# Kernel tuning notes

Measured on AMD Instinct MI355X. Metric: run time of the kernel, lower is better.

The kernel has to match this reference:

```python
import jax, jax.numpy as jnp
import numpy as np

N_NODES, N_EDGES = 512, 4096
P_OBJ, P_REL = 512, 256
D_NODE = D_EDGE = 256
H_GNN = 512
N_LAYERS = 2
N_OBJ_CLS, N_REL_CLS = 160, 26


def _pointnet(x, w1, b1, w2, b2, w3, b3):
    # x: [B, C_in, P] point cloud; pointwise conv1d == per-point MLP, then max-pool over points
    h = jax.nn.relu(jnp.einsum('bcp,cd->bpd', x, w1) + b1)
    h = jax.nn.relu(jnp.einsum('bpc,cd->bpd', h, w2) + b2)
    h = jnp.einsum('bpc,cd->bpd', h, w3) + b3
    return h.max(axis=1)  # [B, D]


def _mlp3(x, w1, b1, w2, b2, w3, b3):
    h = jax.nn.relu(x @ w1 + b1)
    h = jax.nn.relu(h @ w2 + b2)
    return h @ w3 + b3


def setup_inputs() -> dict:
    key = jax.random.key(0)
    ks = iter(jax.random.split(key, 64))

    def w(shape):
        fan = shape[-2]
        return jax.random.normal(next(ks), shape, dtype=jnp.float32) / np.float32(np.sqrt(fan))

    def b(shape):
        return jnp.zeros(shape, jnp.float32)

    d3 = 2 * D_NODE + D_EDGE  # triplet concat dim
    inp = dict(
        obj_points=jax.random.normal(next(ks), (N_NODES, 3, P_OBJ), dtype=jnp.float32),
        rel_points=jax.random.normal(next(ks), (N_EDGES, 4, P_REL), dtype=jnp.float32),
        edge_index=jax.random.randint(next(ks), (2, N_EDGES), 0, N_NODES),
        obj_w1=w((3, 64)), obj_b1=b((64,)), obj_w2=w((64, 128)), obj_b2=b((128,)),
        obj_w3=w((128, D_NODE)), obj_b3=b((D_NODE,)),
        rel_w1=w((4, 64)), rel_b1=b((64,)), rel_w2=w((64, 128)), rel_b2=b((128,)),
        rel_w3=w((128, D_EDGE)), rel_b3=b((D_EDGE,)),
        g_tw1=w((N_LAYERS, d3, H_GNN)), g_tb1=b((N_LAYERS, H_GNN)),
        g_tw2=w((N_LAYERS, H_GNN, d3)), g_tb2=b((N_LAYERS, d3)),
        g_nw1=w((N_LAYERS, D_NODE, H_GNN)), g_nb1=b((N_LAYERS, H_GNN)),
        g_nw2=w((N_LAYERS, H_GNN, D_NODE)), g_nb2=b((N_LAYERS, D_NODE)),
        oc_w1=w((D_NODE, 512)), oc_b1=b((512,)), oc_w2=w((512, 256)), oc_b2=b((256,)),
        oc_w3=w((256, N_OBJ_CLS)), oc_b3=b((N_OBJ_CLS,)),
        rc_w1=w((D_EDGE, 512)), rc_b1=b((512,)), rc_w2=w((512, 256)), rc_b2=b((256,)),
        rc_w3=w((256, N_REL_CLS)), rc_b3=b((N_REL_CLS,)),
    )
    return inp


def reference(obj_points, rel_points, edge_index,
              obj_w1, obj_b1, obj_w2, obj_b2, obj_w3, obj_b3,
              rel_w1, rel_b1, rel_w2, rel_b2, rel_w3, rel_b3,
              g_tw1, g_tb1, g_tw2, g_tb2, g_nw1, g_nb1, g_nw2, g_nb2,
              oc_w1, oc_b1, oc_w2, oc_b2, oc_w3, oc_b3,
              rc_w1, rc_b1, rc_w2, rc_b2, rc_w3, rc_b3):
    # PointNet encoders
    x = _pointnet(obj_points, obj_w1, obj_b1, obj_w2, obj_b2, obj_w3, obj_b3)  # [N, Dn]
    e = _pointnet(rel_points, rel_w1, rel_b1, rel_w2, rel_b2, rel_w3, rel_b3)  # [E, De]
    s, o = edge_index[0], edge_index[1]
    ones = jnp.ones((N_EDGES, 1), x.dtype)
    # Triplet GNN (GraphTripleConv-style message passing)
    for l in range(N_LAYERS):
        t = jnp.concatenate([x[s], e, x[o]], axis=-1)                 # [E, 2Dn+De]
        h = jax.nn.relu(t @ g_tw1[l] + g_tb1[l]) @ g_tw2[l] + g_tb2[l]
        ns = h[:, :D_NODE]
        ne = h[:, D_NODE:D_NODE + D_EDGE]
        no = h[:, D_NODE + D_EDGE:]
        pooled = (jax.ops.segment_sum(ns, s, num_segments=N_NODES)
                  + jax.ops.segment_sum(no, o, num_segments=N_NODES))
        cnt = (jax.ops.segment_sum(ones, s, num_segments=N_NODES)
               + jax.ops.segment_sum(ones, o, num_segments=N_NODES))
        avg = pooled / jnp.maximum(cnt, 1.0)                          # scatter-mean
        x = jax.nn.relu(avg @ g_nw1[l] + g_nb1[l]) @ g_nw2[l] + g_nb2[l]
        e = ne
    obj_cls = jax.nn.log_softmax(
        _mlp3(x, oc_w1, oc_b1, oc_w2, oc_b2, oc_w3, oc_b3), axis=-1)  # PointNetCls
    rel_cls = jax.nn.sigmoid(
        _mlp3(e, rc_w1, rc_b1, rc_w2, rc_b2, rc_w3, rc_b3))           # PointNetRelClsMulti
    return (obj_cls, rel_cls)
```

## Files before the change

kernel.cpp:

```cpp
#include <hip/hip_runtime.h>
#include <hip/hip_bf16.h>
#include <math.h>

#define N_NODES 512
#define N_EDGES 4096
#define D_NODE 256
#define D3 768
#define H_GNN 512
#define N_OBJ_CLS 160
#define N_REL_CLS 26

typedef __attribute__((ext_vector_type(8))) short bf16x8;
typedef __attribute__((ext_vector_type(4))) float f32x4;

__device__ __forceinline__ unsigned short f2bf(float x) {
  unsigned u = __float_as_uint(x);
  u = u + 0x7FFFu + ((u >> 16) & 1u);
  return (unsigned short)(u >> 16);
}
__device__ __forceinline__ float bf2f(unsigned short h) {
  return __uint_as_float(((unsigned)h) << 16);
}
__device__ __forceinline__ unsigned cvtpk(float a, float b) {
  __hip_bfloat162 h = __float22bfloat162_rn(make_float2(a, b));
  return *reinterpret_cast<unsigned*>(&h);
}

struct WEnt { const float* src; unsigned short* dh; unsigned short* dl; int K; int N; int start; };
struct WBatch { WEnt e[18]; int total; };

__global__ __launch_bounds__(256) void wtrans_batch(WBatch wb) {
  int idx = blockIdx.x * 256 + threadIdx.x;
  const int stride = gridDim.x * 256;
  for (; idx < wb.total; idx += stride) {
    int i = 0;
#pragma unroll
    for (int t = 1; t < 18; ++t) if (idx >= wb.e[t].start) i = t;
    const int local = idx - wb.e[i].start;
    const int K = wb.e[i].K;
    const int n = local / K, k = local - n * K;
    const float v = wb.e[i].src[k * wb.e[i].N + n];
    const unsigned short hi = f2bf(v);
    wb.e[i].dh[local] = hi;
    wb.e[i].dl[local] = f2bf(v - bf2f(hi));
  }
}

template<int CIN, int PTOT, int NSPLIT>
__global__ __launch_bounds__(256) void pointnet_mfma(
    const float* __restrict__ in,
    const float* __restrict__ w1, const float* __restrict__ b1,
    const unsigned short* __restrict__ w2t, const float* __restrict__ b2,
    const unsigned short* __restrict__ w3t, const float* __restrict__ b3,
    unsigned short* __restrict__ outh,
    float* __restrict__ pmax)
{
  constexpr int PBLK = PTOT / NSPLIT;
  __shared__ unsigned short h1h[64][72];
  __shared__ unsigned short h2h[64][136];
  const int tid = threadIdx.x;
  const int wv = tid >> 6, l = tid & 63, lr = l & 15, lg = l >> 4;
  const int blk = blockIdx.x;
  const int b  = blk / NSPLIT;
  const int sp = blk % NSPLIT;
  const float* inb = in + (size_t)b * CIN * PTOT + (size_t)sp * PBLK;

  const int chA = 2 * (l & 31);
  const int sub = l >> 5;
  float w1c0[CIN], w1c1[CIN];
#pragma unroll
  for (int c = 0; c < CIN; ++c) {
    w1c0[c] = w1[c * 64 + chA];
    w1c1[c] = w1[c * 64 + chA + 1];
  }
  const float b1v0 = b1[chA], b1v1 = b1[chA + 1];

  bf16x8 w2f[2][2];
#pragma unroll
  for (int mt = 0; mt < 2; ++mt)
#pragma unroll
    for (int kt = 0; kt < 2; ++kt)
      w2f[mt][kt] = *(const bf16x8*)(w2t + (size_t)(32 * wv + mt * 16 + lr) * 64 + kt * 32 + lg * 8);
  bf16x8 w3f[4][4];
#pragma unroll
  for (int mt = 0; mt < 4; ++mt)
#pragma unroll
    for (int kt = 0; kt < 4; ++kt)
      w3f[mt][kt] = *(const bf16x8*)(w3t + (size_t)(64 * wv + mt * 16 + lr) * 128 + kt * 32 + lg * 8);

  float4 b2v[2];
#pragma unroll
  for (int mt = 0; mt < 2; ++mt)
    b2v[mt] = *(const float4*)&b2[32 * wv + mt * 16 + lg * 4];

  f32x4 mxf[4];
#pragma unroll
  for (int mt = 0; mt < 4; ++mt) { f32x4 z = {-INFINITY, -INFINITY, -INFINITY, -INFINITY}; mxf[mt] = z; }

  for (int t0 = 0; t0 < PBLK; t0 += 64) {
    {
      const int pl0 = wv * 16 + sub * 8;
      float4 xv0[CIN], xv1[CIN];
#pragma unroll
      for (int c = 0; c < CIN; ++c) {
        xv0[c] = *(const float4*)&inb[c * PTOT + t0 + pl0];
        xv1[c] = *(const float4*)&inb[c * PTOT + t0 + pl0 + 4];
      }
#pragma unroll
      for (int pp = 0; pp < 8; ++pp) {
        float a0 = b1v0, a1 = b1v1;
#pragma unroll
        for (int c = 0; c < CIN; ++c) {
          const float xc = (pp < 4) ? ((const float*)&xv0[c])[pp]
                                    : ((const float*)&xv1[c])[pp - 4];
          a0 = fmaf(xc, w1c0[c], a0);
          a1 = fmaf(xc, w1c1[c], a1);
        }
        a0 = fmaxf(a0, 0.f); a1 = fmaxf(a1, 0.f);
        *(unsigned*)&h1h[pl0 + pp][chA] = cvtpk(a0, a1);
      }
    }
    __syncthreads();
#pragma unroll
    for (int ntt = 0; ntt < 4; ++ntt) {
      bf16x8 bh[2];
#pragma unroll
      for (int kt = 0; kt < 2; ++kt)
        bh[kt] = *(const bf16x8*)&h1h[ntt * 16 + lr][kt * 32 + lg * 8];
#pragma unroll
      for (int mt = 0; mt < 2; ++mt) {
        f32x4 a = {0.f, 0.f, 0.f, 0.f};
#pragma unroll
        for (int kt = 0; kt < 2; ++kt)
          a = __builtin_amdgcn_mfma_f32_16x16x32_bf16(w2f[mt][kt], bh[kt], a, 0, 0, 0);
        const float v0 = fmaxf(a[0] + b2v[mt].x, 0.f);
        const float v1 = fmaxf(a[1] + b2v[mt].y, 0.f);
        const float v2 = fmaxf(a[2] + b2v[mt].z, 0.f);
        const float v3 = fmaxf(a[3] + b2v[mt].w, 0.f);
        const int pr = ntt * 16 + lr, cc = 32 * wv + mt * 16 + lg * 4;
        *(uint2*)&h2h[pr][cc] = make_uint2(cvtpk(v0, v1), cvtpk(v2, v3));
      }
    }
    __syncthreads();
#pragma unroll
    for (int ntt = 0; ntt < 4; ++ntt) {
      bf16x8 ah[4];
#pragma unroll
      for (int kt = 0; kt < 4; ++kt)
        ah[kt] = *(const bf16x8*)&h2h[ntt * 16 + lr][kt * 32 + lg * 8];
#pragma unroll
      for (int mt = 0; mt < 4; ++mt) {
        f32x4 a = {0.f, 0.f, 0.f, 0.f};
#pragma unroll
        for (int kt = 0; kt < 4; ++kt)
          a = __builtin_amdgcn_mfma_f32_16x16x32_bf16(w3f[mt][kt], ah[kt], a, 0, 0, 0);
#pragma unroll
        for (int j = 0; j < 4; ++j) mxf[mt][j] = fmaxf(mxf[mt][j], a[j]);
      }
    }
    __syncthreads();
  }
#pragma unroll
  for (int mt = 0; mt < 4; ++mt)
#pragma unroll
    for (int j = 0; j < 4; ++j) {
      float v = mxf[mt][j];
      v = fmaxf(v, __shfl_xor(v, 1));
      v = fmaxf(v, __shfl_xor(v, 2));
      v = fmaxf(v, __shfl_xor(v, 4));
      v = fmaxf(v, __shfl_xor(v, 8));
      mxf[mt][j] = v;
    }
  if (lr == 0) {
    if (NSPLIT == 1) {
#pragma unroll
      for (int mt = 0; mt < 4; ++mt) {
        const int ch = 64 * wv + mt * 16 + lg * 4;
        const float4 b3v = *(const float4*)&b3[ch];
        const size_t o = (size_t)b * 256 + ch;
        *(uint2*)(outh + o) = make_uint2(cvtpk(mxf[mt][0] + b3v.x, mxf[mt][1] + b3v.y),
                                         cvtpk(mxf[mt][2] + b3v.z, mxf[mt][3] + b3v.w));
      }
    } else {
#pragma unroll
      for (int mt = 0; mt < 4; ++mt) {
        const int ch = 64 * wv + mt * 16 + lg * 4;
        const size_t o = ((size_t)b * NSPLIT + sp) * 256 + ch;
        *(float4*)&pmax[o] = make_float4(mxf[mt][0], mxf[mt][1], mxf[mt][2], mxf[mt][3]);
      }
    }
  }
}

template<int NSPLIT>
__global__ __launch_bounds__(256) void combine_max(
    const float* __restrict__ pmax, const float* __restrict__ b3,
    unsigned short* __restrict__ outh)
{
  const int b = blockIdx.x, ch = threadIdx.x;
  float m = pmax[(size_t)b * NSPLIT * 256 + ch];
#pragma unroll
  for (int s = 1; s < NSPLIT; ++s)
    m = fmaxf(m, pmax[((size_t)b * NSPLIT + s) * 256 + ch]);
  outh[(size_t)b * 256 + ch] = f2bf(m + b3[ch]);
}

template<int ACT, int OUT, bool GATHER>
__global__ __launch_bounds__(256) void mgemm(
    const unsigned short* __restrict__ Ah, int lda,
    const unsigned short* __restrict__ Eh,
    const int* __restrict__ ei,
    const unsigned short* __restrict__ Wh, const unsigned short* __restrict__ Wl,
    const float* __restrict__ bias,
    unsigned short* __restrict__ Oh, int ldo,
    float* __restrict__ Of, float* __restrict__ pooled,
    int M, int N, int K)
{
  __shared__ unsigned short sAh[64][40];
  __shared__ unsigned short sBh[64][40], sBl[64][40];
  __shared__ int sS[64], sO[64];
  const int tid = threadIdx.x;
  const int wv = tid >> 6, l = tid & 63, lr = l & 15, lg = l >> 4;
  const int wm = wv >> 1, wn = wv & 1;
  const int bm = blockIdx.y * 64, bn = blockIdx.x * 64;
  const int srow = tid >> 2, sch = (tid & 3) * 8;

  if ((GATHER || OUT == 2) && tid < 64) {
    sS[tid] = ei[bm + tid];
    sO[tid] = ei[N_EDGES + bm + tid];
  }

  float bv[2];
#pragma unroll
  for (int ni = 0; ni < 2; ++ni) {
    const int col = bn + wn * 32 + ni * 16 + lr;
    bv[ni] = (col < N) ? bias[col] : 0.f;
  }

  f32x4 acc[2][2];
#pragma unroll
  for (int mi = 0; mi < 2; ++mi)
#pragma unroll
    for (int ni = 0; ni < 2; ++ni) { f32x4 z = {0.f, 0.f, 0.f, 0.f}; acc[mi][ni] = z; }

  for (int k0 = 0; k0 < K; k0 += 32) {
    __syncthreads();
    {
      const unsigned short* ph;
      if (GATHER) {
        const int kg = k0 + sch;
        if (kg < 256)      ph = Ah + (size_t)sS[srow] * 256 + kg;
        else if (kg < 512) ph = Eh + (size_t)(bm + srow) * 256 + (kg - 256);
        else               ph = Ah + (size_t)sO[srow] * 256 + (kg - 512);
      } else {
        ph = Ah + (size_t)(bm + srow) * lda + k0 + sch;
      }
      *(bf16x8*)&sAh[srow][sch] = *(const bf16x8*)ph;
    }
    {
      const int n = bn + srow;
      bf16x8 vh = {0,0,0,0,0,0,0,0}, vl = {0,0,0,0,0,0,0,0};
      if (n < N) {
        const size_t o = (size_t)n * K + k0 + sch;
        vh = *(const bf16x8*)(Wh + o);
        vl = *(const bf16x8*)(Wl + o);
      }
      *(bf16x8*)&sBh[srow][sch] = vh;
      *(bf16x8*)&sBl[srow][sch] = vl;
    }
    __syncthreads();
    bf16x8 afh[2], bfh[2], bfl[2];
#pragma unroll
    for (int mi = 0; mi < 2; ++mi)
      afh[mi] = *(const bf16x8*)&sAh[wm * 32 + mi * 16 + lr][lg * 8];
#pragma unroll
    for (int ni = 0; ni < 2; ++ni) {
      bfh[ni] = *(const bf16x8*)&sBh[wn * 32 + ni * 16 + lr][lg * 8];
      bfl[ni] = *(const bf16x8*)&sBl[wn * 32 + ni * 16 + lr][lg * 8];
    }
#pragma unroll
    for (int mi = 0; mi < 2; ++mi)
#pragma unroll
      for (int ni = 0; ni < 2; ++ni) {
        acc[mi][ni] = __builtin_amdgcn_mfma_f32_16x16x32_bf16(afh[mi], bfh[ni], acc[mi][ni], 0, 0, 0);
        acc[mi][ni] = __builtin_amdgcn_mfma_f32_16x16x32_bf16(afh[mi], bfl[ni], acc[mi][ni], 0, 0, 0);
      }
  }
#pragma unroll
  for (int mi = 0; mi < 2; ++mi)
#pragma unroll
    for (int ni = 0; ni < 2; ++ni) {
      const int colb = bn + wn * 32 + ni * 16 + lr;
#pragma unroll
      for (int j = 0; j < 4; ++j) {
        const int lrow = wm * 32 + mi * 16 + lg * 4 + j;
        float v = acc[mi][ni][j] + bv[ni];
        if (ACT == 1) v = fmaxf(v, 0.f);
        else if (ACT == 2) v = 1.f / (1.f + expf(-v));
        if (OUT == 0) {
          if (colb < N) Oh[(size_t)(bm + lrow) * ldo + colb] = f2bf(v);
        } else if (OUT == 1) {
          if (colb < N) Of[(size_t)(bm + lrow) * ldo + colb] = v;
        } else {
          if (colb < 256) {
            atomicAdd(&pooled[(size_t)sS[lrow] * 256 + colb], v);
          } else if (colb < 512) {
            Oh[(size_t)(bm + lrow) * 256 + (colb - 256)] = f2bf(v);
          } else {
            atomicAdd(&pooled[(size_t)sO[lrow] * 256 + (colb - 512)], v);
          }
        }
      }
    }
}

__global__ __launch_bounds__(256) void count_kernel(const int* __restrict__ ei,
                                                    float* __restrict__ cnt)
{
  const int i = blockIdx.x * blockDim.x + threadIdx.x;
  if (i < 2 * N_EDGES) atomicAdd(&cnt[ei[i]], 1.0f);
}

__global__ __launch_bounds__(256) void avg_plane_kernel(const float* __restrict__ pooled,
                                                        const float* __restrict__ cnt,
                                                        unsigned short* __restrict__ ah)
{
  const int i = blockIdx.x * 256 + threadIdx.x;
  ah[i] = f2bf(pooled[i] / fmaxf(cnt[i >> 8], 1.0f));
}

__global__ __launch_bounds__(256) void logsoftmax_kernel(const float* __restrict__ logits,
                                                         float* __restrict__ out)
{
  __shared__ float red[256];
  const int r = blockIdx.x, tid = threadIdx.x;
  const float v = (tid < N_OBJ_CLS) ? logits[(size_t)r * N_OBJ_CLS + tid] : -INFINITY;
  red[tid] = v;
  __syncthreads();
  for (int s = 128; s > 0; s >>= 1) {
    if (tid < s) red[tid] = fmaxf(red[tid], red[tid + s]);
    __syncthreads();
  }
  const float mxv = red[0];
  __syncthreads();
  red[tid] = (tid < N_OBJ_CLS) ? expf(v - mxv) : 0.0f;
  __syncthreads();
  for (int s = 128; s > 0; s >>= 1) {
    if (tid < s) red[tid] += red[tid + s];
    __syncthreads();
  }
  const float lse = mxv + logf(red[0]);
  if (tid < N_OBJ_CLS) out[(size_t)r * N_OBJ_CLS + tid] = v - lse;
}

extern "C" void kernel_launch(void* const* d_in, const int* in_sizes, int n_in,
                              void* d_out, int out_size, void* d_ws, size_t ws_size,
                              hipStream_t stream)
{
  const float* obj_points = (const float*)d_in[0];
  const float* rel_points = (const float*)d_in[1];
  const int*   edge_index = (const int*)d_in[2];
  const float* obj_w1 = (const float*)d_in[3];
  const float* obj_b1 = (const float*)d_in[4];
  const float* obj_w2 = (const float*)d_in[5];
  const float* obj_b2 = (const float*)d_in[6];
  const float* obj_w3 = (const float*)d_in[7];
  const float* obj_b3 = (const float*)d_in[8];
  const float* rel_w1 = (const float*)d_in[9];
  const float* rel_b1 = (const float*)d_in[10];
  const float* rel_w2 = (const float*)d_in[11];
  const float* rel_b2 = (const float*)d_in[12];
  const float* rel_w3 = (const float*)d_in[13];
  const float* rel_b3 = (const float*)d_in[14];
  const float* g_tw1 = (const float*)d_in[15];
  const float* g_tb1 = (const float*)d_in[16];
  const float* g_tw2 = (const float*)d_in[17];
  const float* g_tb2 = (const float*)d_in[18];
  const float* g_nw1 = (const float*)d_in[19];
  const float* g_nb1 = (const float*)d_in[20];
  const float* g_nw2 = (const float*)d_in[21];
  const float* g_nb2 = (const float*)d_in[22];
  const float* oc_w1 = (const float*)d_in[23];
  const float* oc_b1 = (const float*)d_in[24];
  const float* oc_w2 = (const float*)d_in[25];
  const float* oc_b2 = (const float*)d_in[26];
  const float* oc_w3 = (const float*)d_in[27];
  const float* oc_b3 = (const float*)d_in[28];
  const float* rc_w1 = (const float*)d_in[29];
  const float* rc_b1 = (const float*)d_in[30];
  const float* rc_w2 = (const float*)d_in[31];
  const float* rc_b2 = (const float*)d_in[32];
  const float* rc_w3 = (const float*)d_in[33];
  const float* rc_b3 = (const float*)d_in[34];
  float* out = (float*)d_out;

  unsigned short* u = (unsigned short*)d_ws;
  size_t uo = 0;
  auto UA = [&](size_t n) { unsigned short* p = u + uo; uo += n; return p; };
  unsigned short* x0h = UA(131072);
  unsigned short* x1h = UA(131072);
  unsigned short* e0h = UA(1048576);
  unsigned short* neh = UA(1048576);
  unsigned short* h1h = UA(2097152);
  unsigned short* avgh = UA(131072);
  unsigned short* nhh = UA(262144);
  unsigned short* ow2h = UA(8192);   unsigned short* ow2l = UA(8192);
  unsigned short* ow3h = UA(32768);  unsigned short* ow3l = UA(32768);
  unsigned short* rw2h = UA(8192);   unsigned short* rw2l = UA(8192);
  unsigned short* rw3h = UA(32768);  unsigned short* rw3l = UA(32768);
  unsigned short* tw1h[2], *tw1l[2], *tw2h[2], *tw2l[2], *nw1h[2], *nw1l[2], *nw2h[2], *nw2l[2];
  for (int i = 0; i < 2; ++i) { tw1h[i] = UA(393216); tw1l[i] = UA(393216); }
  for (int i = 0; i < 2; ++i) { tw2h[i] = UA(393216); tw2l[i] = UA(393216); }
  for (int i = 0; i < 2; ++i) { nw1h[i] = UA(131072); nw1l[i] = UA(131072); }
  for (int i = 0; i < 2; ++i) { nw2h[i] = UA(131072); nw2l[i] = UA(131072); }
  unsigned short* oc1h = UA(131072); unsigned short* oc1l = UA(131072);
  unsigned short* oc2h = UA(131072); unsigned short* oc2l = UA(131072);
  unsigned short* oc3h = UA(40960);  unsigned short* oc3l = UA(40960);
  unsigned short* rc1h = UA(131072); unsigned short* rc1l = UA(131072);
  unsigned short* rc2h = UA(131072); unsigned short* rc2l = UA(131072);
  unsigned short* rc3h = UA(6656);   unsigned short* rc3l = UA(6656);
  float* f = (float*)(u + ((uo + 7) & ~(size_t)7));
  float* pooled = f;
  float* cntf   = f + 131072;
  float* logits = f + 131584;
  float* pmax   = f + 213504;
  unsigned short* hh1h = h1h;
  unsigned short* hh2h = e0h;

  WBatch wb;
  int cum = 0, wi = 0;
  auto ADD = [&](const float* src, unsigned short* dh, unsigned short* dl, int K, int N) {
    wb.e[wi].src = src; wb.e[wi].dh = dh; wb.e[wi].dl = dl;
    wb.e[wi].K = K; wb.e[wi].N = N; wb.e[wi].start = cum;
    cum += K * N; ++wi;
  };
  ADD(obj_w2, ow2h, ow2l, 64, 128);
  ADD(obj_w3, ow3h, ow3l, 128, 256);
  ADD(rel_w2, rw2h, rw2l, 64, 128);
  ADD(rel_w3, rw3h, rw3l, 128, 256);
  for (int i = 0; i < 2; ++i) ADD(g_tw1 + (size_t)i * 393216, tw1h[i], tw1l[i], 768, 512);
  for (int i = 0; i < 2; ++i) ADD(g_tw2 + (size_t)i * 393216, tw2h[i], tw2l[i], 512, 768);
  for (int i = 0; i < 2; ++i) ADD(g_nw1 + (size_t)i * 131072, nw1h[i], nw1l[i], 256, 512);
  for (int i = 0; i < 2; ++i) ADD(g_nw2 + (size_t)i * 131072, nw2h[i], nw2l[i], 512, 256);
  ADD(oc_w1, oc1h, oc1l, 256, 512);
  ADD(oc_w2, oc2h, oc2l, 512, 256);
  ADD(oc_w3, oc3h, oc3l, 256, 160);
  ADD(rc_w1, rc1h, rc1l, 256, 512);
  ADD(rc_w2, rc2h, rc2l, 512, 256);
  ADD(rc_w3, rc3h, rc3l, 256, 26);
  wb.total = cum;
  wtrans_batch<<<4096, 256, 0, stream>>>(wb);

  pointnet_mfma<3, 512, 4><<<N_NODES * 4, 256, 0, stream>>>(
      obj_points, obj_w1, obj_b1, ow2h, obj_b2, ow3h, obj_b3, nullptr, pmax);
  combine_max<4><<<N_NODES, 256, 0, stream>>>(pmax, obj_b3, x0h);
  pointnet_mfma<4, 256, 1><<<N_EDGES, 256, 0, stream>>>(
      rel_points, rel_w1, rel_b1, rw2h, rel_b2, rw3h, rel_b3, e0h, nullptr);

  hipMemsetAsync(cntf, 0, 512 * sizeof(float), stream);
  count_kernel<<<32, 256, 0, stream>>>(edge_index, cntf);

  unsigned short *xch = x0h, *xnh = x1h;
  unsigned short *ech = e0h;
  for (int ll = 0; ll < 2; ++ll) {
    mgemm<1, 0, true><<<dim3(8, 64), 256, 0, stream>>>(
        xch, 256, ech, edge_index, tw1h[ll], tw1l[ll], g_tb1 + ll * H_GNN,
        h1h, 512, nullptr, nullptr, N_EDGES, H_GNN, D3);
    hipMemsetAsync(pooled, 0, (size_t)N_NODES * D_NODE * sizeof(float), stream);
    mgemm<0, 2, false><<<dim3(12, 64), 256, 0, stream>>>(
        h1h, 512, nullptr, edge_index, tw2h[ll], tw2l[ll], g_tb2 + ll * D3,
        neh, 256, nullptr, pooled, N_EDGES, D3, H_GNN);
    avg_plane_kernel<<<512, 256, 0, stream>>>(pooled, cntf, avgh);
    mgemm<1, 0, false><<<dim3(8, 8), 256, 0, stream>>>(
        avgh, 256, nullptr, nullptr, nw1h[ll], nw1l[ll], g_nb1 + ll * H_GNN,
        nhh, 512, nullptr, nullptr, N_NODES, H_GNN, D_NODE);
    mgemm<0, 0, false><<<dim3(4, 8), 256, 0, stream>>>(
        nhh, 512, nullptr, nullptr, nw2h[ll], nw2l[ll], g_nb2 + ll * D_NODE,
        xnh, 256, nullptr, nullptr, N_NODES, D_NODE, H_GNN);
    unsigned short* t = xch; xch = xnh; xnh = t;
    ech = neh;
  }

  mgemm<1, 0, false><<<dim3(8, 8), 256, 0, stream>>>(
      xch, 256, nullptr, nullptr, oc1h, oc1l, oc_b1,
      hh1h, 512, nullptr, nullptr, N_NODES, 512, 256);
  mgemm<1, 0, false><<<dim3(4, 8), 256, 0, stream>>>(
      hh1h, 512, nullptr, nullptr, oc2h, oc2l, oc_b2,
      hh2h, 256, nullptr, nullptr, N_NODES, 256, 512);
  mgemm<0, 1, false><<<dim3(3, 8), 256, 0, stream>>>(
      hh2h, 256, nullptr, nullptr, oc3h, oc3l, oc_b3,
      nullptr, N_OBJ_CLS, logits, nullptr, N_NODES, N_OBJ_CLS, 256);
  logsoftmax_kernel<<<N_NODES, 256, 0, stream>>>(logits, out);

  mgemm<1, 0, false><<<dim3(8, 64), 256, 0, stream>>>(
      ech, 256, nullptr, nullptr, rc1h, rc1l, rc_b1,
      hh1h, 512, nullptr, nullptr, N_EDGES, 512, 256);
  mgemm<1, 0, false><<<dim3(4, 64), 256, 0, stream>>>(
      hh1h, 512, nullptr, nullptr, rc2h, rc2l, rc_b2,
      hh2h, 256, nullptr, nullptr, N_EDGES, 256, 512);
  mgemm<2, 1, false><<<dim3(1, 64), 256, 0, stream>>>(
      hh2h, 256, nullptr, nullptr, rc3h, rc3l, rc_b3,
      nullptr, N_REL_CLS, out + (size_t)N_NODES * N_OBJ_CLS, nullptr,
      N_EDGES, N_REL_CLS, 256);
}
```

Baseline: 342.7 us.

## Prefetch next K-tile into registers and widen GEMM K step to 64

The MFMA GEMM kernel now processes 64 K-elements per shared-memory stage instead of 32. It also software-pipelines the global loads: the next tile is fetched into registers while MFMAs run on the current tile in shared memory. This is meant to hide global load latency and halve the number of barrier pairs per K. In exchange it uses more registers and shared memory, and it requires K to be a multiple of 64.

```diff
diff --git a/kernel.cpp b/kernel.cpp
--- a/kernel.cpp
+++ b/kernel.cpp
@@ -216,19 +216,21 @@
     float* __restrict__ Of, float* __restrict__ pooled,
     int M, int N, int K)
 {
-  __shared__ unsigned short sAh[64][40];
-  __shared__ unsigned short sBh[64][40], sBl[64][40];
+  __shared__ unsigned short sAh[64][72];
+  __shared__ unsigned short sBh[64][72], sBl[64][72];
   __shared__ int sS[64], sO[64];
   const int tid = threadIdx.x;
   const int wv = tid >> 6, l = tid & 63, lr = l & 15, lg = l >> 4;
   const int wm = wv >> 1, wn = wv & 1;
   const int bm = blockIdx.y * 64, bn = blockIdx.x * 64;
-  const int srow = tid >> 2, sch = (tid & 3) * 8;
+  const int srow = tid >> 3;
+  const int sch  = (tid & 7) * 8;
 
   if ((GATHER || OUT == 2) && tid < 64) {
     sS[tid] = ei[bm + tid];
     sO[tid] = ei[N_EDGES + bm + tid];
   }
+  __syncthreads();
 
   float bv[2];
 #pragma unroll
@@ -243,48 +245,72 @@
 #pragma unroll
     for (int ni = 0; ni < 2; ++ni) { f32x4 z = {0.f, 0.f, 0.f, 0.f}; acc[mi][ni] = z; }
 
-  for (int k0 = 0; k0 < K; k0 += 32) {
-    __syncthreads();
-    {
-      const unsigned short* ph;
-      if (GATHER) {
-        const int kg = k0 + sch;
-        if (kg < 256)      ph = Ah + (size_t)sS[srow] * 256 + kg;
-        else if (kg < 512) ph = Eh + (size_t)(bm + srow) * 256 + (kg - 256);
-        else               ph = Ah + (size_t)sO[srow] * 256 + (kg - 512);
-      } else {
-        ph = Ah + (size_t)(bm + srow) * lda + k0 + sch;
-      }
-      *(bf16x8*)&sAh[srow][sch] = *(const bf16x8*)ph;
-    }
-    {
-      const int n = bn + srow;
-      bf16x8 vh = {0,0,0,0,0,0,0,0}, vl = {0,0,0,0,0,0,0,0};
-      if (n < N) {
-        const size_t o = (size_t)n * K + k0 + sch;
-        vh = *(const bf16x8*)(Wh + o);
-        vl = *(const bf16x8*)(Wl + o);
-      }
-      *(bf16x8*)&sBh[srow][sch] = vh;
-      *(bf16x8*)&sBl[srow][sch] = vl;
-    }
-    __syncthreads();
-    bf16x8 afh[2], bfh[2], bfl[2];
-#pragma unroll
-    for (int mi = 0; mi < 2; ++mi)
-      afh[mi] = *(const bf16x8*)&sAh[wm * 32 + mi * 16 + lr][lg * 8];
-#pragma unroll
-    for (int ni = 0; ni < 2; ++ni) {
-      bfh[ni] = *(const bf16x8*)&sBh[wn * 32 + ni * 16 + lr][lg * 8];
-      bfl[ni] = *(const bf16x8*)&sBl[wn * 32 + ni * 16 + lr][lg * 8];
-    }
-#pragma unroll
-    for (int mi = 0; mi < 2; ++mi)
+  const int nsteps = K >> 6;
+
+  auto loadA = [&](int k0, int it) -> bf16x8 {
+    const int r = it * 32 + srow;
+    const unsigned short* ph;
+    if (GATHER) {
+      const int kg = k0 + sch;
+      if (kg < 256)      ph = Ah + (size_t)sS[r] * 256 + kg;
+      else if (kg < 512) ph = Eh + (size_t)(bm + r) * 256 + (kg - 256);
+      else               ph = Ah + (size_t)sO[r] * 256 + (kg - 512);
+    } else {
+      ph = Ah + (size_t)(bm + r) * lda + k0 + sch;
+    }
+    return *(const bf16x8*)ph;
+  };
+  auto loadB = [&](const unsigned short* W, int k0, int it) -> bf16x8 {
+    int n = bn + it * 32 + srow;
+    if (n >= N) n = N - 1;
+    return *(const bf16x8*)(W + (size_t)n * K + k0 + sch);
+  };
+
+  bf16x8 rA[2], rBh[2], rBl[2];
+#pragma unroll
+  for (int it = 0; it < 2; ++it) {
+    rA[it]  = loadA(0, it);
+    rBh[it] = loadB(Wh, 0, it);
+    rBl[it] = loadB(Wl, 0, it);
+  }
+
+  for (int t = 0; t < nsteps; ++t) {
+    __syncthreads();
+#pragma unroll
+    for (int it = 0; it < 2; ++it) {
+      *(bf16x8*)&sAh[it * 32 + srow][sch] = rA[it];
+      *(bf16x8*)&sBh[it * 32 + srow][sch] = rBh[it];
+      *(bf16x8*)&sBl[it * 32 + srow][sch] = rBl[it];
+    }
+    __syncthreads();
+    if (t + 1 < nsteps) {
+      const int k1 = (t + 1) << 6;
+#pragma unroll
+      for (int it = 0; it < 2; ++it) {
+        rA[it]  = loadA(k1, it);
+        rBh[it] = loadB(Wh, k1, it);
+        rBl[it] = loadB(Wl, k1, it);
+      }
+    }
+#pragma unroll
+    for (int kt = 0; kt < 2; ++kt) {
+      bf16x8 afh[2], bfh[2], bfl[2];
+#pragma unroll
+      for (int mi = 0; mi < 2; ++mi)
+        afh[mi] = *(const bf16x8*)&sAh[wm * 32 + mi * 16 + lr][kt * 32 + lg * 8];
 #pragma unroll
       for (int ni = 0; ni < 2; ++ni) {
-        acc[mi][ni] = __builtin_amdgcn_mfma_f32_16x16x32_bf16(afh[mi], bfh[ni], acc[mi][ni], 0, 0, 0);
-        acc[mi][ni] = __builtin_amdgcn_mfma_f32_16x16x32_bf16(afh[mi], bfl[ni], acc[mi][ni], 0, 0, 0);
-      }
+        bfh[ni] = *(const bf16x8*)&sBh[wn * 32 + ni * 16 + lr][kt * 32 + lg * 8];
+        bfl[ni] = *(const bf16x8*)&sBl[wn * 32 + ni * 16 + lr][kt * 32 + lg * 8];
+      }
+#pragma unroll
+      for (int mi = 0; mi < 2; ++mi)
+#pragma unroll
+        for (int ni = 0; ni < 2; ++ni) {
+          acc[mi][ni] = __builtin_amdgcn_mfma_f32_16x16x32_bf16(afh[mi], bfh[ni], acc[mi][ni], 0, 0, 0);
+          acc[mi][ni] = __builtin_amdgcn_mfma_f32_16x16x32_bf16(afh[mi], bfl[ni], acc[mi][ni], 0, 0, 0);
+        }
+    }
   }
 #pragma unroll
   for (int mi = 0; mi < 2; ++mi)
```

New measurement: 294.0 us. -14.2%, faster.
